# Performance work log

Measured on AMD Instinct MI355X. Metric: run time of the kernel, lower is better.

Reference implementation:

```python
import jax, jax.numpy as jnp
import numpy as np

V = 1_000_000   # sparse_id_num
D = 64          # embedding_dim
F = 26          # sparse_feature_cnt
L = 8           # ids per feature bag (fixed-size ragged regularization)
B = 4096        # batch
IN_DIM = F * D  # 1664
HIDDENS = (1024, 1024, 512)


def setup_inputs() -> dict:
    key = jax.random.key(0)
    ks = jax.random.split(key, 4 + 4 * len(HIDDENS))
    inp = {}
    inp["x"] = jax.random.randint(ks[0], (B, F, L), 0, V, dtype=jnp.int64)
    inp["emb_table"] = jax.random.normal(ks[1], (V, D), dtype=jnp.float32) * 0.01
    ki = 2
    for i, h in enumerate(HIDDENS):
        inp[f"w1_{i}"] = jax.random.normal(ks[ki], (IN_DIM, h), dtype=jnp.float32) * 0.02
        inp[f"b1_{i}"] = jnp.zeros((h,), dtype=jnp.float32)
        inp[f"w2_{i}"] = jax.random.normal(ks[ki + 1], (h, IN_DIM), dtype=jnp.float32) * 0.02
        inp[f"b2_{i}"] = jnp.zeros((IN_DIM,), dtype=jnp.float32)
        ki += 2
    inp["lin_w"] = jax.random.normal(ks[ki], (IN_DIM, 1), dtype=jnp.float32) * 0.02
    inp["lin_b"] = jnp.zeros((1,), dtype=jnp.float32)
    return inp


def reference(x, emb_table,
              w1_0, b1_0, w2_0, b2_0,
              w1_1, b1_1, w2_1, b2_1,
              w1_2, b1_2, w2_2, b2_2,
              lin_w, lin_b):
    # Batched embedding lookup + sum-pool over bag dim + concat over features.
    # x: [B, F, L] -> gather [B, F, L, D] -> sum over L -> [B, F, D] -> [B, F*D]
    pooled = emb_table[x].sum(axis=2)              # [B, F, D]
    feat = pooled.reshape(x.shape[0], -1)          # [B, F*D]
    # Residual blocks: relu(linear2(relu(linear1(x))) + x)
    for w1, b1, w2, b2 in ((w1_0, b1_0, w2_0, b2_0),
                           (w1_1, b1_1, w2_1, b2_1),
                           (w1_2, b1_2, w2_2, b2_2)):
        h = jax.nn.relu(feat @ w1 + b1)
        feat = jax.nn.relu(h @ w2 + b2 + feat)
    return jax.nn.sigmoid(feat @ lin_w + lin_b)    # [B, 1]
```

## Files before the change

### kernel.cpp

```cpp
#include <hip/hip_runtime.h>
#include <hip/hip_bf16.h>

#define BATCH 4096
#define FEATS 26
#define BAG   8
#define EDIM  64
#define INDIM 1664

typedef short bf16x8 __attribute__((ext_vector_type(8)));
typedef float f32x4  __attribute__((ext_vector_type(4)));
typedef unsigned short u16x8 __attribute__((ext_vector_type(8)));

__device__ __forceinline__ unsigned short f2bf(float f) {
    unsigned u = __float_as_uint(f);
    unsigned r = (u + 0x7FFFu + ((u >> 16) & 1u)) >> 16;
    return (unsigned short)r;
}
__device__ __forceinline__ float bf2f(unsigned short h) {
    return __uint_as_float((unsigned)h << 16);
}
__device__ __forceinline__ void async_cp16(const void* g, void* lds_base_uniform) {
    __builtin_amdgcn_global_load_lds(
        (const __attribute__((address_space(1))) unsigned int*)g,
        (__attribute__((address_space(3))) unsigned int*)lds_base_uniform,
        16, 0, 0);
}

__global__ __launch_bounds__(256) void transpose_to_bf16(
    const float* __restrict__ in, unsigned short* __restrict__ out, int R, int C)
{
    __shared__ unsigned short tile[64][65];
    const int c0 = blockIdx.x * 64, r0 = blockIdx.y * 64;
    const int t = threadIdx.x;
    const int tc = t & 63, tr = t >> 6;
#pragma unroll
    for (int i = 0; i < 16; ++i) {
        int r = tr + i * 4;
        tile[r][tc] = f2bf(in[(long long)(r0 + r) * C + c0 + tc]);
    }
    __syncthreads();
    const int wr = t >> 3, wc = t & 7;
#pragma unroll
    for (int half = 0; half < 2; ++half) {
        int row = wr + half * 32;
        u16x8 v;
#pragma unroll
        for (int j = 0; j < 8; ++j) v[j] = tile[wc * 8 + j][row];
        *(u16x8*)(out + (long long)(c0 + row) * R + r0 + wc * 8) = v;
    }
}

__global__ __launch_bounds__(256) void embed_pool(
    const int* __restrict__ x, const float* __restrict__ emb,
    unsigned short* __restrict__ feat)
{
    int bag  = blockIdx.x * 4 + (threadIdx.x >> 6);
    int lane = threadIdx.x & 63;
    int b = bag / FEATS;
    int f = bag - b * FEATS;
    const int* xs = x + (long long)bag * BAG;
    float s = 0.f;
#pragma unroll
    for (int l = 0; l < BAG; ++l) {
        int id = xs[l];
        s += emb[(long long)id * EDIM + lane];
    }
    feat[(long long)b * INDIM + f * EDIM + lane] = f2bf(s);
}

__global__ __launch_bounds__(256) void gemm_bf16(
    const unsigned short* __restrict__ A, const unsigned short* __restrict__ Wt,
    const float* __restrict__ bias, const unsigned short* __restrict__ res,
    unsigned short* __restrict__ out, int M, int N, int K, int do_relu)
{
    __shared__ unsigned short As[128 * 32];
    __shared__ unsigned short Bs[128 * 32];

    const int t    = threadIdx.x;
    const int bCol = blockIdx.x * 128;
    const int bRow = blockIdx.y * 128;
    const int wave = t >> 6, lane = t & 63;
    const int wm = wave & 1, wn = wave >> 1;
    const int lm = lane & 15, quad = lane >> 4;

    const int srow = (lane >> 2);
    const int sk   = (lane & 3) * 8;

    f32x4 acc[4][4] = {};

    for (int kt = 0; kt < K; kt += 32) {
#pragma unroll
        for (int it = 0; it < 2; ++it) {
            int c = wave * 2 + it;
            int row = c * 16 + srow;
            async_cp16(A  + (long long)(bRow + row) * K + kt + sk, As + c * 512);
            async_cp16(Wt + (long long)(bCol + row) * K + kt + sk, Bs + c * 512);
        }
        __syncthreads();

        bf16x8 a[4], b[4];
#pragma unroll
        for (int i = 0; i < 4; ++i)
            a[i] = *(const bf16x8*)&As[(wm * 64 + i * 16 + lm) * 32 + quad * 8];
#pragma unroll
        for (int j = 0; j < 4; ++j)
            b[j] = *(const bf16x8*)&Bs[(wn * 64 + j * 16 + lm) * 32 + quad * 8];
#pragma unroll
        for (int i = 0; i < 4; ++i)
#pragma unroll
            for (int j = 0; j < 4; ++j)
                acc[i][j] = __builtin_amdgcn_mfma_f32_16x16x32_bf16(
                    a[i], b[j], acc[i][j], 0, 0, 0);
        __syncthreads();
    }

#pragma unroll
    for (int i = 0; i < 4; ++i) {
#pragma unroll
        for (int j = 0; j < 4; ++j) {
            int col = bCol + wn * 64 + j * 16 + lm;
            float bv = bias[col];
#pragma unroll
            for (int r = 0; r < 4; ++r) {
                int row = bRow + wm * 64 + i * 16 + quad * 4 + r;
                float v = acc[i][j][r] + bv;
                if (res) v += bf2f(res[(long long)row * N + col]);
                if (do_relu) v = fmaxf(v, 0.f);
                out[(long long)row * N + col] = f2bf(v);
            }
        }
    }
}

__global__ __launch_bounds__(256) void final_head(
    const unsigned short* __restrict__ feat, const float* __restrict__ lin_w,
    const float* __restrict__ lin_b, float* __restrict__ out)
{
    int row  = blockIdx.x * 4 + (threadIdx.x >> 6);
    int lane = threadIdx.x & 63;
    const unsigned short* fr = feat + (long long)row * INDIM;
    float s = 0.f;
#pragma unroll
    for (int it = 0; it < INDIM / 64; ++it)
        s += bf2f(fr[it * 64 + lane]) * lin_w[it * 64 + lane];
#pragma unroll
    for (int off = 32; off; off >>= 1)
        s += __shfl_down(s, off, 64);
    if (lane == 0)
        out[row] = 1.f / (1.f + __expf(-(s + lin_b[0])));
}

extern "C" void kernel_launch(void* const* d_in, const int* in_sizes, int n_in,
                              void* d_out, int out_size, void* d_ws, size_t ws_size,
                              hipStream_t stream) {
    const int*   x    = (const int*)  d_in[0];
    const float* emb  = (const float*)d_in[1];
    const float* w1_0 = (const float*)d_in[2];
    const float* b1_0 = (const float*)d_in[3];
    const float* w2_0 = (const float*)d_in[4];
    const float* b2_0 = (const float*)d_in[5];
    const float* w1_1 = (const float*)d_in[6];
    const float* b1_1 = (const float*)d_in[7];
    const float* w2_1 = (const float*)d_in[8];
    const float* b2_1 = (const float*)d_in[9];
    const float* w1_2 = (const float*)d_in[10];
    const float* b1_2 = (const float*)d_in[11];
    const float* w2_2 = (const float*)d_in[12];
    const float* b2_2 = (const float*)d_in[13];
    const float* linw = (const float*)d_in[14];
    const float* linb = (const float*)d_in[15];
    float* out = (float*)d_out;

    unsigned short* feat = (unsigned short*)d_ws;
    unsigned short* h    = feat + (long long)BATCH * INDIM;
    unsigned short* p    = h + (long long)BATCH * 1024;
    unsigned short* w1_0t = p; p += 1024 * INDIM;
    unsigned short* w2_0t = p; p += INDIM * 1024;
    unsigned short* w1_1t = p; p += 1024 * INDIM;
    unsigned short* w2_1t = p; p += INDIM * 1024;
    unsigned short* w1_2t = p; p += 512 * INDIM;
    unsigned short* w2_2t = p; p += INDIM * 512;

    transpose_to_bf16<<<dim3(1024/64, INDIM/64), 256, 0, stream>>>(w1_0, w1_0t, INDIM, 1024);
    transpose_to_bf16<<<dim3(INDIM/64, 1024/64), 256, 0, stream>>>(w2_0, w2_0t, 1024, INDIM);
    transpose_to_bf16<<<dim3(1024/64, INDIM/64), 256, 0, stream>>>(w1_1, w1_1t, INDIM, 1024);
    transpose_to_bf16<<<dim3(INDIM/64, 1024/64), 256, 0, stream>>>(w2_1, w2_1t, 1024, INDIM);
    transpose_to_bf16<<<dim3(512/64,  INDIM/64), 256, 0, stream>>>(w1_2, w1_2t, INDIM, 512);
    transpose_to_bf16<<<dim3(INDIM/64, 512/64),  256, 0, stream>>>(w2_2, w2_2t, 512, INDIM);

    embed_pool<<<BATCH * FEATS / 4, 256, 0, stream>>>(x, emb, feat);

    gemm_bf16<<<dim3(1024/128, BATCH/128), 256, 0, stream>>>(
        feat, w1_0t, b1_0, nullptr, h, BATCH, 1024, INDIM, 1);
    gemm_bf16<<<dim3(INDIM/128, BATCH/128), 256, 0, stream>>>(
        h, w2_0t, b2_0, feat, feat, BATCH, INDIM, 1024, 1);
    gemm_bf16<<<dim3(1024/128, BATCH/128), 256, 0, stream>>>(
        feat, w1_1t, b1_1, nullptr, h, BATCH, 1024, INDIM, 1);
    gemm_bf16<<<dim3(INDIM/128, BATCH/128), 256, 0, stream>>>(
        h, w2_1t, b2_1, feat, feat, BATCH, INDIM, 1024, 1);
    gemm_bf16<<<dim3(512/128, BATCH/128), 256, 0, stream>>>(
        feat, w1_2t, b1_2, nullptr, h, BATCH, 512, INDIM, 1);
    gemm_bf16<<<dim3(INDIM/128, BATCH/128), 256, 0, stream>>>(
        h, w2_2t, b2_2, feat, feat, BATCH, INDIM, 512, 1);

    final_head<<<BATCH / 4, 256, 0, stream>>>(feat, linw, linb, out);
}
```

Measured before the change: 647.0 us.

## Multi-buffer GEMM LDS loads with async prefetch, 8 waves and swizzled LDS

Rewrites the bf16 MFMA GEMM main loop to use a 4-deep ring of LDS buffers. Async global-to-LDS loads are issued two tiles ahead and throttled with vmcnt waits and a single barrier per k-step, replacing the load/sync/compute/sync pattern. The block grows to 512 threads (8 waves, each computing 64x32), and k-chunks are XOR-swizzled in LDS to avoid bank conflicts on fragment reads. The cost is a larger LDS footprint (64 KB per block), which may limit blocks per CU, plus hand-written waitcnt encodings that are fragile.

```diff
diff --git a/kernel.cpp b/kernel.cpp
--- a/kernel.cpp
+++ b/kernel.cpp
@@ -25,6 +25,7 @@
         (__attribute__((address_space(3))) unsigned int*)lds_base_uniform,
         16, 0, 0);
 }
+#define WAITCNT_VM(n) __builtin_amdgcn_s_waitcnt(0x0F70 | (n))
 
 __global__ __launch_bounds__(256) void transpose_to_bf16(
     const float* __restrict__ in, unsigned short* __restrict__ out, int R, int C)
@@ -68,13 +69,14 @@
     feat[(long long)b * INDIM + f * EDIM + lane] = f2bf(s);
 }
 
-__global__ __launch_bounds__(256) void gemm_bf16(
+#define NBUF 4
+__global__ __launch_bounds__(512) void gemm_bf16(
     const unsigned short* __restrict__ A, const unsigned short* __restrict__ Wt,
     const float* __restrict__ bias, const unsigned short* __restrict__ res,
     unsigned short* __restrict__ out, int M, int N, int K, int do_relu)
 {
-    __shared__ unsigned short As[128 * 32];
-    __shared__ unsigned short Bs[128 * 32];
+    __shared__ unsigned short As[NBUF * 128 * 32];
+    __shared__ unsigned short Bs[NBUF * 128 * 32];
 
     const int t    = threadIdx.x;
     const int bCol = blockIdx.x * 128;
@@ -83,42 +85,65 @@
     const int wm = wave & 1, wn = wave >> 1;
     const int lm = lane & 15, quad = lane >> 4;
 
-    const int srow = (lane >> 2);
-    const int sk   = (lane & 3) * 8;
-
-    f32x4 acc[4][4] = {};
-
-    for (int kt = 0; kt < K; kt += 32) {
-#pragma unroll
-        for (int it = 0; it < 2; ++it) {
-            int c = wave * 2 + it;
-            int row = c * 16 + srow;
-            async_cp16(A  + (long long)(bRow + row) * K + kt + sk, As + c * 512);
-            async_cp16(Wt + (long long)(bCol + row) * K + kt + sk, Bs + c * 512);
-        }
-        __syncthreads();
-
-        bf16x8 a[4], b[4];
-#pragma unroll
-        for (int i = 0; i < 4; ++i)
-            a[i] = *(const bf16x8*)&As[(wm * 64 + i * 16 + lm) * 32 + quad * 8];
-#pragma unroll
-        for (int j = 0; j < 4; ++j)
-            b[j] = *(const bf16x8*)&Bs[(wn * 64 + j * 16 + lm) * 32 + quad * 8];
-#pragma unroll
-        for (int i = 0; i < 4; ++i)
-#pragma unroll
-            for (int j = 0; j < 4; ++j)
-                acc[i][j] = __builtin_amdgcn_mfma_f32_16x16x32_bf16(
-                    a[i], b[j], acc[i][j], 0, 0, 0);
-        __syncthreads();
-    }
+    const int srow = lane >> 2;
+    const int sq   = (lane & 3) ^ ((lane >> 3) & 3);
+    const unsigned short* Ag = A  + (long long)(bRow + wave * 16 + srow) * K + sq * 8;
+    const unsigned short* Bg = Wt + (long long)(bCol + wave * 16 + srow) * K + sq * 8;
+    unsigned short* AsW = As + wave * 512;
+    unsigned short* BsW = Bs + wave * 512;
+
+    const int T = K / 32;
+    f32x4 acc[4][2] = {};
+
+    const int slot = (quad ^ ((lm >> 1) & 3)) * 8;
+
+#define ISSUE(tile_)  do { int _b = (tile_) & (NBUF - 1);                         \
+        async_cp16(Ag + (long long)(tile_) * 32, AsW + _b * 4096);                \
+        async_cp16(Bg + (long long)(tile_) * 32, BsW + _b * 4096); } while (0)
+
+#define COMPUTE(tile_) do { int _b = (tile_) & (NBUF - 1);                        \
+        const unsigned short* _a = As + _b * 4096;                                \
+        const unsigned short* _bp = Bs + _b * 4096;                               \
+        bf16x8 af[4], bf[2];                                                      \
+        _Pragma("unroll")                                                         \
+        for (int i = 0; i < 4; ++i)                                               \
+            af[i] = *(const bf16x8*)&_a[(wm * 64 + i * 16 + lm) * 32 + slot];     \
+        _Pragma("unroll")                                                         \
+        for (int j = 0; j < 2; ++j)                                               \
+            bf[j] = *(const bf16x8*)&_bp[(wn * 32 + j * 16 + lm) * 32 + slot];    \
+        _Pragma("unroll")                                                         \
+        for (int i = 0; i < 4; ++i)                                               \
+            _Pragma("unroll")                                                     \
+            for (int j = 0; j < 2; ++j)                                           \
+                acc[i][j] = __builtin_amdgcn_mfma_f32_16x16x32_bf16(              \
+                    af[i], bf[j], acc[i][j], 0, 0, 0); } while (0)
+
+    ISSUE(0);
+    ISSUE(1);
+    for (int tt = 0; tt < T - 2; ++tt) {
+        ISSUE(tt + 2);
+        WAITCNT_VM(4);
+        asm volatile("" ::: "memory");
+        __builtin_amdgcn_s_barrier();
+        asm volatile("" ::: "memory");
+        COMPUTE(tt);
+    }
+    WAITCNT_VM(2);
+    asm volatile("" ::: "memory");
+    __builtin_amdgcn_s_barrier();
+    asm volatile("" ::: "memory");
+    COMPUTE(T - 2);
+    WAITCNT_VM(0);
+    asm volatile("" ::: "memory");
+    __builtin_amdgcn_s_barrier();
+    asm volatile("" ::: "memory");
+    COMPUTE(T - 1);
 
 #pragma unroll
     for (int i = 0; i < 4; ++i) {
 #pragma unroll
-        for (int j = 0; j < 4; ++j) {
-            int col = bCol + wn * 64 + j * 16 + lm;
+        for (int j = 0; j < 2; ++j) {
+            int col = bCol + wn * 32 + j * 16 + lm;
             float bv = bias[col];
 #pragma unroll
             for (int r = 0; r < 4; ++r) {
@@ -130,6 +155,8 @@
             }
         }
     }
+#undef ISSUE
+#undef COMPUTE
 }
 
 __global__ __launch_bounds__(256) void final_head(
@@ -190,17 +217,17 @@
 
     embed_pool<<<BATCH * FEATS / 4, 256, 0, stream>>>(x, emb, feat);
 
-    gemm_bf16<<<dim3(1024/128, BATCH/128), 256, 0, stream>>>(
+    gemm_bf16<<<dim3(1024/128, BATCH/128), 512, 0, stream>>>(
         feat, w1_0t, b1_0, nullptr, h, BATCH, 1024, INDIM, 1);
-    gemm_bf16<<<dim3(INDIM/128, BATCH/128), 256, 0, stream>>>(
+    gemm_bf16<<<dim3(INDIM/128, BATCH/128), 512, 0, stream>>>(
         h, w2_0t, b2_0, feat, feat, BATCH, INDIM, 1024, 1);
-    gemm_bf16<<<dim3(1024/128, BATCH/128), 256, 0, stream>>>(
+    gemm_bf16<<<dim3(1024/128, BATCH/128), 512, 0, stream>>>(
         feat, w1_1t, b1_1, nullptr, h, BATCH, 1024, INDIM, 1);
-    gemm_bf16<<<dim3(INDIM/128, BATCH/128), 256, 0, stream>>>(
+    gemm_bf16<<<dim3(INDIM/128, BATCH/128), 512, 0, stream>>>(
         h, w2_1t, b2_1, feat, feat, BATCH, INDIM, 1024, 1);
-    gemm_bf16<<<dim3(512/128, BATCH/128), 256, 0, stream>>>(
+    gemm_bf16<<<dim3(512/128, BATCH/128), 512, 0, stream>>>(
         feat, w1_2t, b1_2, nullptr, h, BATCH, 512, INDIM, 1);
-    gemm_bf16<<<dim3(INDIM/128, BATCH/128), 256, 0, stream>>>(
+    gemm_bf16<<<dim3(INDIM/128, BATCH/128), 512, 0, stream>>>(
         h, w2_2t, b2_2, feat, feat, BATCH, INDIM, 512, 1);
 
     final_head<<<BATCH / 4, 256, 0, stream>>>(feat, linw, linb, out);
```

Result: faster. 565.4 us (-12.6%).
